# Performance work log

Measured on AMD Instinct MI355X. Metric: run time of the kernel, lower is better.

Reference implementation:

```python
import jax, jax.numpy as jnp
import numpy as np
import math

N_QUBITS = 8
EMBED_DIM = 8
NUM_HEADS = 2
N_QLAYERS = 2
TWO_PI = 2.0 * math.pi


def _apply_rx(state, theta, wire):
    # state: (N,) + (2,)*n complex64; theta: scalar or (N,)
    n = state.ndim - 1
    ax = 1 + wire
    a0 = jnp.take(state, 0, axis=ax)
    a1 = jnp.take(state, 1, axis=ax)
    half = jnp.asarray(theta) * 0.5
    c = jnp.cos(half)
    s = jnp.sin(half)
    if c.ndim:  # per-sample angle -> broadcast over remaining qubit axes
        bshape = (-1,) + (1,) * (n - 1)
        c = c.reshape(bshape)
        s = s.reshape(bshape)
    js = 1j * s
    n0 = c * a0 - js * a1
    n1 = -js * a0 + c * a1
    return jnp.stack([n0, n1], axis=ax)


def _apply_cnot(state, ctrl, tgt):
    ac, at = 1 + ctrl, 1 + tgt
    s0 = jnp.take(state, 0, axis=ac)
    s1 = jnp.take(state, 1, axis=ac)
    at2 = at - 1 if at > ac else at  # target axis index after removing control axis
    s1 = jnp.flip(s1, axis=at2)
    return jnp.stack([s0, s1], axis=ac)


def qnode(inputs, weights):
    """AngleEmbedding(RX) + BasicEntanglerLayers(RX + CNOT ring), PauliZ expvals.
    inputs: (N, n) angles; weights: (L, n). Returns (N, n) expvals, fully batched."""
    N, n = inputs.shape
    L = weights.shape[0]
    state = jnp.zeros((N,) + (2,) * n, jnp.complex64)
    state = state.at[(slice(None),) + (0,) * n].set(1.0)
    for i in range(n):  # AngleEmbedding: RX(inputs[:, i]) on wire i
        state = _apply_rx(state, inputs[:, i], i)
    for l in range(L):  # BasicEntanglerLayers
        for i in range(n):
            state = _apply_rx(state, weights[l, i], i)
        for i in range(n):
            state = _apply_cnot(state, i, (i + 1) % n)
    probs = (state.real ** 2 + state.imag ** 2).reshape(N, 2 ** n)
    # wire 0 is the most significant bit of the flattened statevector index
    idx = jnp.arange(2 ** n)
    bits = (idx[:, None] >> jnp.arange(n - 1, -1, -1)[None, :]) & 1  # (2^n, n)
    signs = (1.0 - 2.0 * bits).astype(probs.dtype)
    return probs @ signs  # (N, n)


def _qproj(x, weights):
    # apply qnode to every (batch, timestep) vector at once (vectorized loop fusion)
    B, S, E = x.shape
    return qnode(x.reshape(B * S, E), weights).reshape(B, S, E)


def _attention_forward(q, k, v, wq_w, wk_w, wv_w, wd_w):
    B, S, E = q.shape
    H, D = NUM_HEADS, EMBED_DIM // NUM_HEADS
    qp = _qproj(q, wq_w)
    kp = _qproj(k, wk_w)
    vp = _qproj(v, wv_w)
    # split heads: (B, H, S, D)
    qh = qp.reshape(B, S, H, D).transpose(0, 2, 1, 3)
    kh = kp.reshape(B, S, H, D).transpose(0, 2, 1, 3)
    vh = vp.reshape(B, S, H, D).transpose(0, 2, 1, 3)
    scores = jnp.einsum('bhqd,bhkd->bhqk', qh, kh) / jnp.sqrt(jnp.asarray(D, qh.dtype))
    attn = jax.nn.softmax(scores, axis=-1)
    ctx = jnp.einsum('bhqk,bhkd->bhqd', attn, vh)
    concat = ctx.transpose(0, 2, 1, 3).reshape(B, S, E)
    out = _qproj(concat, wd_w)
    return out, attn


def setup_inputs() -> dict:
    key = jax.random.key(0)
    kq, kk, kv, k1, k2, k3, k4 = jax.random.split(key, 7)
    B, S, E = 32, 1024, EMBED_DIM
    return {
        'q': jax.random.normal(kq, (B, S, E), jnp.float32),
        'k': jax.random.normal(kk, (B, S, E), jnp.float32),
        'v': jax.random.normal(kv, (B, S, E), jnp.float32),
        'wq_weights': jax.random.uniform(k1, (N_QLAYERS, N_QUBITS), jnp.float32) * TWO_PI,
        'wk_weights': jax.random.uniform(k2, (N_QLAYERS, N_QUBITS), jnp.float32) * TWO_PI,
        'wv_weights': jax.random.uniform(k3, (N_QLAYERS, N_QUBITS), jnp.float32) * TWO_PI,
        'dense_weights': jax.random.uniform(k4, (N_QLAYERS, N_QUBITS), jnp.float32) * TWO_PI,
    }


def reference(q, k, v, wq_weights, wk_weights, wv_weights, dense_weights):
    return _attention_forward(q, k, v, wq_weights, wk_weights, wv_weights, dense_weights)
```

## Files before the change

### kernel.cpp

```cpp
#include <hip/hip_runtime.h>
#include <math.h>


#define NSAMP 32768

typedef float f2 __attribute__((ext_vector_type(2)));

#define QX1 0xB1
#define QX2 0x4E
#define QX3 0x1B
#define QB0 0x00
#define QB1 0x55
#define QB2 0xAA
#define QB3 0xFF
#define ROW_MIRROR 0x140
#define ROW_HALF_MIRROR 0x141

template <int CTRL>
__device__ __forceinline__ float dppf(float x) {
  int xi = __float_as_int(x);
  return __int_as_float(
      __builtin_amdgcn_update_dpp(xi, xi, CTRL, 0xF, 0xF, false));
}

template <int CTRL>
__device__ __forceinline__ f2 dpp2(f2 v) {
  f2 r;
  r.x = dppf<CTRL>(v.x);
  r.y = dppf<CTRL>(v.y);
  return r;
}

__device__ __forceinline__ f2 swap2(f2 v) {
  f2 r;
  r.x = v.y;
  r.y = v.x;
  return r;
}

#define F2FMA(a, b, c) __builtin_elementwise_fma((a), (b), (c))


template <int CTRL>
__device__ __forceinline__ void gq0(float c, float s, f2* vr, f2* vi) {
  const f2 c2 = {c, c}, s2 = {s, s};
#pragma unroll
  for (int m = 0; m < 32; ++m) {
    f2 pr = dpp2<CTRL>(vr[m]);
    f2 pi = dpp2<CTRL>(vi[m]);
    vr[m] = F2FMA(c2, vr[m], s2 * pi);
    vi[m] = F2FMA(c2, vi[m], -s2 * pr);
  }
}

template <int CTRL>
__device__ __forceinline__ void gq_l1(float c, float s, f2* vr, f2* vi) {
  const f2 c2 = {c, c}, s2 = {s, s};
#pragma unroll
  for (int m = 0; m < 32; m += 2) {
    f2 pr0 = dpp2<CTRL>(vr[m]), pi0 = dpp2<CTRL>(vi[m]);
    f2 pr1 = dpp2<CTRL>(vr[m + 1]), pi1 = dpp2<CTRL>(vi[m + 1]);
    vr[m] = F2FMA(c2, vr[m], s2 * pi1);
    vi[m] = F2FMA(c2, vi[m], -s2 * pr1);
    vr[m + 1] = F2FMA(c2, vr[m + 1], s2 * pi0);
    vi[m + 1] = F2FMA(c2, vi[m + 1], -s2 * pr0);
  }
}

template <int CTRL>
__device__ __forceinline__ void gq_l20(float c, float s, f2* vr, f2* vi) {
  const f2 c2 = {c, c}, s2 = {s, s};
#pragma unroll
  for (int m = 0; m < 32; ++m) {
    f2 pr = dpp2<CTRL>(vr[m]);
    f2 pi = dpp2<CTRL>(vi[m]);
    vr[m] = F2FMA(c2, vr[m], s2 * swap2(pi));
    vi[m] = F2FMA(c2, vi[m], -s2 * swap2(pr));
  }
}

template <int ML>
__device__ __forceinline__ void gl(float c, float s, f2* vr, f2* vi) {
  constexpr int HB = ML >= 16 ? 16 : ML >= 8 ? 8 : ML >= 4 ? 4
                     : ML >= 2 ? 2 : 1;
  const f2 c2 = {c, c}, s2 = {s, s};
#pragma unroll
  for (int m = 0; m < 32; ++m) {
    if (!(m & HB)) {
      const int p = m ^ ML;
      f2 a0r = vr[m], a0i = vi[m], a1r = vr[p], a1i = vi[p];
      vr[m] = F2FMA(c2, a0r, s2 * a1i);
      vi[m] = F2FMA(c2, a0i, -s2 * a1r);
      vr[p] = F2FMA(c2, a1r, s2 * a0i);
      vi[p] = F2FMA(c2, a1i, -s2 * a0r);
    }
  }
}

__device__ __forceinline__ void gl20(float c, float s, f2* vr, f2* vi) {
  const f2 c2 = {c, c}, s2 = {s, s};
#pragma unroll
  for (int m = 0; m < 32; ++m) {
    f2 orr = vr[m], oii = vi[m];
    vr[m] = F2FMA(c2, orr, s2 * swap2(oii));
    vi[m] = F2FMA(c2, oii, -s2 * swap2(orr));
  }
}

__device__ __forceinline__ void gl30(float c, float s, f2* vr, f2* vi) {
  const f2 c2 = {c, c}, s2 = {s, s};
#pragma unroll
  for (int m = 0; m < 32; ++m) {
    if (!(m & 0x10)) {
      const int p = m ^ 0x10;
      f2 or0 = vr[m], oi0 = vi[m], or1 = vr[p], oi1 = vi[p];
      vr[m] = F2FMA(c2, or0, s2 * swap2(oi1));
      vi[m] = F2FMA(c2, oi0, -s2 * swap2(or1));
      vr[p] = F2FMA(c2, or1, s2 * swap2(oi0));
      vi[p] = F2FMA(c2, oi1, -s2 * swap2(or0));
    }
  }
}

__device__ __forceinline__ float quad_wht(float v, int qq) {
  float u = dppf<QX1>(v);
  v = (qq & 1) ? (u - v) : (v + u);
  u = dppf<QX2>(v);
  v = (qq & 2) ? (u - v) : (v + u);
  return v;
}

__device__ __forceinline__ void qsim_wave(const float* __restrict__ in,
                                          float* __restrict__ outp,
                                          int sampBase,
                                          const float* __restrict__ wc,
                                          const float* __restrict__ wsn) {
  const int lane = threadIdx.x & 63;
  const int qq = lane & 3;
  const int g = lane >> 2;
  const int samp = sampBase + g;

  const float2 xx = *(const float2*)(in + (size_t)samp * 8 + 2 * qq);
  float h0 = 0.5f * xx.x, h1 = 0.5f * xx.y;
  float c0 = cosf(h0), s0 = sinf(h0);
  float c1 = cosf(h1), s1 = sinf(h1);
  float cw[8], sw[8];
  cw[0] = dppf<QB0>(c0); cw[1] = dppf<QB0>(c1);
  sw[0] = dppf<QB0>(s0); sw[1] = dppf<QB0>(s1);
  cw[2] = dppf<QB1>(c0); cw[3] = dppf<QB1>(c1);
  sw[2] = dppf<QB1>(s0); sw[3] = dppf<QB1>(s1);
  cw[4] = dppf<QB2>(c0); cw[5] = dppf<QB2>(c1);
  sw[4] = dppf<QB2>(s0); sw[5] = dppf<QB2>(s1);
  cw[6] = dppf<QB3>(c0); cw[7] = dppf<QB3>(c1);
  sw[6] = dppf<QB3>(s0); sw[7] = dppf<QB3>(s1);

  float mm[32];
  mm[0] = ((qq & 1) ? sw[1] : cw[1]) * ((qq & 2) ? sw[0] : cw[0]);
#pragma unroll
  for (int k = 0; k < 5; ++k) {
    const float cc = cw[7 - k], ss = sw[7 - k];
#pragma unroll
    for (int t = (1 << k) - 1; t >= 0; --t) {
      mm[t + (1 << k)] = mm[t] * ss;
      mm[t] = mm[t] * cc;
    }
  }

  f2 vr[32], vi[32];
  const int pq = __builtin_popcount(qq);
#pragma unroll
  for (int m = 0; m < 32; ++m) {
    const float mx = mm[m] * cw[2];
    const float my = mm[m] * sw[2];
    const int plx = __builtin_popcount(m) & 3;
    f2 r, i;
    if (plx == 0) { r.x = mx;    i.x = 0.0f;  r.y = 0.0f;  i.y = -my; }
    else if (plx == 1) { r.x = 0.0f; i.x = -mx; r.y = -my; i.y = 0.0f; }
    else if (plx == 2) { r.x = -mx; i.x = 0.0f; r.y = 0.0f; i.y = my; }
    else { r.x = 0.0f; i.x = mx;   r.y = my;   i.y = 0.0f; }
    vr[m] = r;
    vi[m] = i;
  }
  if (pq == 1) {
#pragma unroll
    for (int m = 0; m < 32; ++m) {
      f2 t = vr[m];
      vr[m] = vi[m];
      vi[m] = -t;
    }
  } else if (pq == 2) {
#pragma unroll
    for (int m = 0; m < 32; ++m) {
      vr[m] = -vr[m];
      vi[m] = -vi[m];
    }
  }

  gq0<QX2>(wc[0], wsn[0], vr, vi);
  gq0<QX1>(wc[1], wsn[1], vr, vi);
  gl20(wc[2], wsn[2], vr, vi);
  gl<0x10>(wc[3], wsn[3], vr, vi);
  gl<0x08>(wc[4], wsn[4], vr, vi);
  gl<0x04>(wc[5], wsn[5], vr, vi);
  gl<0x02>(wc[6], wsn[6], vr, vi);
  gl<0x01>(wc[7], wsn[7], vr, vi);
  gq0<QX3>(wc[8], wsn[8], vr, vi);
  gq_l20<QX1>(wc[9], wsn[9], vr, vi);
  gl30(wc[10], wsn[10], vr, vi);
  gl<0x18>(wc[11], wsn[11], vr, vi);
  gl<0x0C>(wc[12], wsn[12], vr, vi);
  gl<0x06>(wc[13], wsn[13], vr, vi);
  gl<0x03>(wc[14], wsn[14], vr, vi);
  gq_l1<QX3>(wc[15], wsn[15], vr, vi);

  f2 wv[32];
#pragma unroll
  for (int m = 0; m < 32; ++m)
    wv[m] = F2FMA(vr[m], vr[m], vi[m] * vi[m]);
#pragma unroll
  for (int gi = 0; gi < 4; ++gi) {
#pragma unroll
    for (int k = 0; k < 3; ++k) {
#pragma unroll
      for (int j = 0; j < 8; ++j) {
        if (!(j & (1 << k))) {
          const int a = gi * 8 + j, b2 = a | (1 << k);
          f2 A = wv[a], B = wv[b2];
          wv[a] = A + B;
          wv[b2] = A - B;
        }
      }
    }
  }
  const f2 aA = (wv[5] + wv[13]) - (wv[21] + wv[29]);
  const f2 aBC = (wv[7] + wv[31]) - (wv[15] + wv[23]);
  const f2 aD = (wv[7] + wv[23]) - (wv[15] + wv[31]);
  const f2 aE = (wv[7] + wv[15]) - (wv[23] + wv[31]);
  const f2 aF = (wv[3] + wv[19]) - (wv[11] + wv[27]);
  const f2 aG = (wv[2] + wv[18]) - (wv[10] + wv[26]);
  const float accA = aA.x + aA.y;
  const float accB = aBC.x - aBC.y;
  const float accC = aBC.x + aBC.y;
  const float accD = aD.x - aD.y;
  const float accE = aE.x + aE.y;
  const float accF = aF.x - aF.y;
  const float accG = aG.x - aG.y;

  const float o15 = quad_wht(accA, qq);
  const float o3F = quad_wht(accB, qq);
  const float o1F = quad_wht(accC, qq);
  const float o2F = quad_wht(accD, qq);
  const float o17 = quad_wht(accE, qq);
  const float o2B = quad_wht(accF, qq);
  const float o2A = quad_wht(accG, qq);

  float* orow = outp + (size_t)samp * 8;
  if (qq == 3) orow[0] = o15;
  if (qq == 2) {
    orow[1] = o3F;
    orow[3] = o2F;
    orow[5] = o2B;
    orow[7] = o2A;
  }
  if (qq == 1) {
    orow[2] = o1F;
    orow[4] = o17;
    orow[6] = o15;
  }
}

__device__ __forceinline__ void weight_trig(const float* __restrict__ w,
                                            float* __restrict__ tc,
                                            float* __restrict__ tsn) {
  if (threadIdx.x < 32) {
    const int a = threadIdx.x & 15;
    const float half = 0.5f * w[a];
    if (threadIdx.x < 16)
      tc[a] = cosf(half);
    else
      tsn[a] = sinf(half);
  }
  __syncthreads();
}

__global__ __launch_bounds__(256, 2) void mhaq_qproj3_kernel(
    const float* __restrict__ q, const float* __restrict__ k,
    const float* __restrict__ v, const float* __restrict__ wq,
    const float* __restrict__ wk, const float* __restrict__ wv,
    float* __restrict__ qp, float* __restrict__ kp, float* __restrict__ vp) {
  __shared__ float tc[16], tsn[16];
  const int wg = blockIdx.x * 4 + (threadIdx.x >> 6);
  const int proj = wg >> 11;
  const float* wsel = proj == 0 ? wq : proj == 1 ? wk : wv;
  weight_trig(wsel, tc, tsn);
  const float* in = proj == 0 ? q : proj == 1 ? k : v;
  float* op = proj == 0 ? qp : proj == 1 ? kp : vp;
  qsim_wave(in, op, (wg & 2047) * 16, tc, tsn);
}

__global__ __launch_bounds__(256, 2) void mhaq_qproj1_kernel(
    const float* __restrict__ ctx, const float* __restrict__ wd,
    float* __restrict__ outp) {
  __shared__ float tc[16], tsn[16];
  weight_trig(wd, tc, tsn);
  const int wg = blockIdx.x * 4 + (threadIdx.x >> 6);
  qsim_wave(ctx, outp, wg * 16, tc, tsn);
}

__device__ __forceinline__ float wred_sum(float v) {
  v += dppf<QX1>(v);
  v += dppf<QX2>(v);
  v += dppf<ROW_HALF_MIRROR>(v);
  v += dppf<ROW_MIRROR>(v);
  v += __shfl_xor(v, 16, 64);
  v += __shfl_xor(v, 32, 64);
  return v;
}
__device__ __forceinline__ float wred_max(float v) {
  v = fmaxf(v, dppf<QX1>(v));
  v = fmaxf(v, dppf<QX2>(v));
  v = fmaxf(v, dppf<ROW_HALF_MIRROR>(v));
  v = fmaxf(v, dppf<ROW_MIRROR>(v));
  v = fmaxf(v, __shfl_xor(v, 16, 64));
  v = fmaxf(v, __shfl_xor(v, 32, 64));
  return v;
}

__global__ __launch_bounds__(256, 2) void mhaq_attn_kernel(
    const float* __restrict__ qp, const float* __restrict__ kp,
    const float* __restrict__ vp, float* __restrict__ ctx,
    float* __restrict__ attn) {
  const int wg = blockIdx.x * 4 + (threadIdx.x >> 6);
  const int bh = wg >> 7;
  const int chunk = wg & 127;
  const int b = bh >> 1, h = bh & 1;
  const int lane = threadIdx.x & 63;

  float4 kreg[16], vreg[16];
  const float* kbase = kp + (size_t)b * 1024 * 8 + h * 4;
  const float* vbase = vp + (size_t)b * 1024 * 8 + h * 4;
#pragma unroll
  for (int t = 0; t < 4; ++t) {
#pragma unroll
    for (int c = 0; c < 4; ++c) {
      const size_t j = (size_t)t * 256 + lane * 4 + c;
      kreg[t * 4 + c] = *(const float4*)(kbase + j * 8);
      vreg[t * 4 + c] = *(const float4*)(vbase + j * 8);
    }
  }

  for (int r = 0; r < 8; ++r) {
    const int i = chunk * 8 + r;
    const float4 qv = *(const float4*)(qp + ((size_t)b * 1024 + i) * 8 + h * 4);
    float e[16];
    float mx = -1e30f;
#pragma unroll
    for (int t = 0; t < 16; ++t) {
      float s = qv.x * kreg[t].x + qv.y * kreg[t].y + qv.z * kreg[t].z +
                qv.w * kreg[t].w;
      s *= 0.5f;
      e[t] = s;
      mx = fmaxf(mx, s);
    }
    mx = wred_max(mx);
    float sum = 0.0f;
#pragma unroll
    for (int t = 0; t < 16; ++t) {
      e[t] = __expf(e[t] - mx);
      sum += e[t];
    }
    sum = wred_sum(sum);
    const float rinv = 1.0f / sum;

    float a0 = 0.f, a1 = 0.f, a2 = 0.f, a3 = 0.f;
    float* arow = attn + ((size_t)(bh * 1024 + i)) * 1024;
#pragma unroll
    for (int t = 0; t < 4; ++t) {
      float p0 = e[4 * t] * rinv, p1 = e[4 * t + 1] * rinv,
            p2 = e[4 * t + 2] * rinv, p3 = e[4 * t + 3] * rinv;
      *(float4*)(arow + t * 256 + lane * 4) = make_float4(p0, p1, p2, p3);
      a0 = fmaf(p0, vreg[4 * t].x, a0);
      a1 = fmaf(p0, vreg[4 * t].y, a1);
      a2 = fmaf(p0, vreg[4 * t].z, a2);
      a3 = fmaf(p0, vreg[4 * t].w, a3);
      a0 = fmaf(p1, vreg[4 * t + 1].x, a0);
      a1 = fmaf(p1, vreg[4 * t + 1].y, a1);
      a2 = fmaf(p1, vreg[4 * t + 1].z, a2);
      a3 = fmaf(p1, vreg[4 * t + 1].w, a3);
      a0 = fmaf(p2, vreg[4 * t + 2].x, a0);
      a1 = fmaf(p2, vreg[4 * t + 2].y, a1);
      a2 = fmaf(p2, vreg[4 * t + 2].z, a2);
      a3 = fmaf(p2, vreg[4 * t + 2].w, a3);
      a0 = fmaf(p3, vreg[4 * t + 3].x, a0);
      a1 = fmaf(p3, vreg[4 * t + 3].y, a1);
      a2 = fmaf(p3, vreg[4 * t + 3].z, a2);
      a3 = fmaf(p3, vreg[4 * t + 3].w, a3);
    }
    a0 = wred_sum(a0);
    a1 = wred_sum(a1);
    a2 = wred_sum(a2);
    a3 = wred_sum(a3);
    if (lane == 0)
      *(float4*)(ctx + ((size_t)b * 1024 + i) * 8 + h * 4) =
          make_float4(a0, a1, a2, a3);
  }
}

extern "C" void kernel_launch(void* const* d_in, const int* in_sizes, int n_in,
                              void* d_out, int out_size, void* d_ws,
                              size_t ws_size, hipStream_t stream) {
  (void)in_sizes; (void)n_in; (void)out_size; (void)ws_size;
  const float* q = (const float*)d_in[0];
  const float* k = (const float*)d_in[1];
  const float* v = (const float*)d_in[2];
  const float* wq = (const float*)d_in[3];
  const float* wk = (const float*)d_in[4];
  const float* wv = (const float*)d_in[5];
  const float* wd = (const float*)d_in[6];
  float* outp = (float*)d_out;
  float* attn = outp + 262144;

  float* wsf = (float*)d_ws;
  float* qp = wsf;
  float* kp = qp + (size_t)NSAMP * 8;
  float* vp = kp + (size_t)NSAMP * 8;
  float* ctx = vp + (size_t)NSAMP * 8;

  hipLaunchKernelGGL(mhaq_qproj3_kernel, dim3(1536), dim3(256), 0, stream, q,
                     k, v, wq, wk, wv, qp, kp, vp);
  hipLaunchKernelGGL(mhaq_attn_kernel, dim3(2048), dim3(256), 0, stream, qp,
                     kp, vp, ctx, attn);
  hipLaunchKernelGGL(mhaq_qproj1_kernel, dim3(512), dim3(256), 0, stream, ctx,
                     wd, outp);
}
```

Before: 364.7 us.

## Split each 8-qubit statevector across 8 lanes instead of 4

Rewrites the quantum-projection simulation so each sample's 256 amplitudes are spread over 8 lanes with 32 scalar complex amplitudes per lane, replacing the 4-lane layout with 64 amplitudes held as float2 pairs. Cross-lane gates now use DPP permutes, including a two-step permute for the third lane bit, and the final Walsh-Hadamard reduction gains a third lane stage. Each lane now computes all eight input cosines and sines itself instead of sharing them through DPP broadcasts. Launch grids double, and launch bounds rise to 4 blocks per SIMD for lower register pressure and higher occupancy. The cost is more DPP traffic and redundant trig per lane. The attention kernel, which likely dominates runtime, is unchanged.

```diff
diff --git a/kernel.cpp b/kernel.cpp
--- a/kernel.cpp
+++ b/kernel.cpp
@@ -3,16 +3,10 @@
 
 
 #define NSAMP 32768
-
-typedef float f2 __attribute__((ext_vector_type(2)));
 
 #define QX1 0xB1
 #define QX2 0x4E
 #define QX3 0x1B
-#define QB0 0x00
-#define QB1 0x55
-#define QB2 0xAA
-#define QB3 0xFF
 #define ROW_MIRROR 0x140
 #define ROW_HALF_MIRROR 0x141
 
@@ -23,110 +17,82 @@
       __builtin_amdgcn_update_dpp(xi, xi, CTRL, 0xF, 0xF, false));
 }
 
+template <int P1>
+__device__ __forceinline__ float dpp2x(float x) {
+  return dppf<ROW_HALF_MIRROR>(dppf<P1>(x));
+}
+
+
 template <int CTRL>
-__device__ __forceinline__ f2 dpp2(f2 v) {
-  f2 r;
-  r.x = dppf<CTRL>(v.x);
-  r.y = dppf<CTRL>(v.y);
-  return r;
-}
-
-__device__ __forceinline__ f2 swap2(f2 v) {
-  f2 r;
-  r.x = v.y;
-  r.y = v.x;
-  return r;
-}
-
-#define F2FMA(a, b, c) __builtin_elementwise_fma((a), (b), (c))
-
-
-template <int CTRL>
-__device__ __forceinline__ void gq0(float c, float s, f2* vr, f2* vi) {
-  const f2 c2 = {c, c}, s2 = {s, s};
+__device__ __forceinline__ void cg1(float c, float s, float* vr, float* vi) {
 #pragma unroll
   for (int m = 0; m < 32; ++m) {
-    f2 pr = dpp2<CTRL>(vr[m]);
-    f2 pi = dpp2<CTRL>(vi[m]);
-    vr[m] = F2FMA(c2, vr[m], s2 * pi);
-    vi[m] = F2FMA(c2, vi[m], -s2 * pr);
-  }
-}
-
-template <int CTRL>
-__device__ __forceinline__ void gq_l1(float c, float s, f2* vr, f2* vi) {
-  const f2 c2 = {c, c}, s2 = {s, s};
-#pragma unroll
-  for (int m = 0; m < 32; m += 2) {
-    f2 pr0 = dpp2<CTRL>(vr[m]), pi0 = dpp2<CTRL>(vi[m]);
-    f2 pr1 = dpp2<CTRL>(vr[m + 1]), pi1 = dpp2<CTRL>(vi[m + 1]);
-    vr[m] = F2FMA(c2, vr[m], s2 * pi1);
-    vi[m] = F2FMA(c2, vi[m], -s2 * pr1);
-    vr[m + 1] = F2FMA(c2, vr[m + 1], s2 * pi0);
-    vi[m + 1] = F2FMA(c2, vi[m + 1], -s2 * pr0);
-  }
-}
-
-template <int CTRL>
-__device__ __forceinline__ void gq_l20(float c, float s, f2* vr, f2* vi) {
-  const f2 c2 = {c, c}, s2 = {s, s};
+    const float pr = dppf<CTRL>(vr[m]);
+    const float pi = dppf<CTRL>(vi[m]);
+    vr[m] = fmaf(c, vr[m], s * pi);
+    vi[m] = fmaf(c, vi[m], -s * pr);
+  }
+}
+
+template <int P1>
+__device__ __forceinline__ void cg2(float c, float s, float* vr, float* vi) {
 #pragma unroll
   for (int m = 0; m < 32; ++m) {
-    f2 pr = dpp2<CTRL>(vr[m]);
-    f2 pi = dpp2<CTRL>(vi[m]);
-    vr[m] = F2FMA(c2, vr[m], s2 * swap2(pi));
-    vi[m] = F2FMA(c2, vi[m], -s2 * swap2(pr));
-  }
-}
-
-template <int ML>
-__device__ __forceinline__ void gl(float c, float s, f2* vr, f2* vi) {
+    const float pr = dpp2x<P1>(vr[m]);
+    const float pi = dpp2x<P1>(vi[m]);
+    vr[m] = fmaf(c, vr[m], s * pi);
+    vi[m] = fmaf(c, vi[m], -s * pr);
+  }
+}
+
+template <int P1, bool TWO, int ML>
+__device__ __forceinline__ void cgl(float c, float s, float* vr, float* vi) {
   constexpr int HB = ML >= 16 ? 16 : ML >= 8 ? 8 : ML >= 4 ? 4
                      : ML >= 2 ? 2 : 1;
-  const f2 c2 = {c, c}, s2 = {s, s};
 #pragma unroll
   for (int m = 0; m < 32; ++m) {
     if (!(m & HB)) {
       const int p = m ^ ML;
-      f2 a0r = vr[m], a0i = vi[m], a1r = vr[p], a1i = vi[p];
-      vr[m] = F2FMA(c2, a0r, s2 * a1i);
-      vi[m] = F2FMA(c2, a0i, -s2 * a1r);
-      vr[p] = F2FMA(c2, a1r, s2 * a0i);
-      vi[p] = F2FMA(c2, a1i, -s2 * a0r);
-    }
-  }
-}
-
-__device__ __forceinline__ void gl20(float c, float s, f2* vr, f2* vi) {
-  const f2 c2 = {c, c}, s2 = {s, s};
+      float prl, pil, prp, pip;
+      if constexpr (TWO) {
+        prl = dpp2x<P1>(vr[p]); pil = dpp2x<P1>(vi[p]);
+        prp = dpp2x<P1>(vr[m]); pip = dpp2x<P1>(vi[m]);
+      } else {
+        prl = dppf<P1>(vr[p]); pil = dppf<P1>(vi[p]);
+        prp = dppf<P1>(vr[m]); pip = dppf<P1>(vi[m]);
+      }
+      vr[m] = fmaf(c, vr[m], s * pil);
+      vi[m] = fmaf(c, vi[m], -s * prl);
+      vr[p] = fmaf(c, vr[p], s * pip);
+      vi[p] = fmaf(c, vi[p], -s * prp);
+    }
+  }
+}
+
+template <int ML>
+__device__ __forceinline__ void gl(float c, float s, float* vr, float* vi) {
+  constexpr int HB = ML >= 16 ? 16 : ML >= 8 ? 8 : ML >= 4 ? 4
+                     : ML >= 2 ? 2 : 1;
 #pragma unroll
   for (int m = 0; m < 32; ++m) {
-    f2 orr = vr[m], oii = vi[m];
-    vr[m] = F2FMA(c2, orr, s2 * swap2(oii));
-    vi[m] = F2FMA(c2, oii, -s2 * swap2(orr));
-  }
-}
-
-__device__ __forceinline__ void gl30(float c, float s, f2* vr, f2* vi) {
-  const f2 c2 = {c, c}, s2 = {s, s};
-#pragma unroll
-  for (int m = 0; m < 32; ++m) {
-    if (!(m & 0x10)) {
-      const int p = m ^ 0x10;
-      f2 or0 = vr[m], oi0 = vi[m], or1 = vr[p], oi1 = vi[p];
-      vr[m] = F2FMA(c2, or0, s2 * swap2(oi1));
-      vi[m] = F2FMA(c2, oi0, -s2 * swap2(or1));
-      vr[p] = F2FMA(c2, or1, s2 * swap2(oi0));
-      vi[p] = F2FMA(c2, oi1, -s2 * swap2(or0));
-    }
-  }
-}
-
-__device__ __forceinline__ float quad_wht(float v, int qq) {
+    if (!(m & HB)) {
+      const int p = m ^ ML;
+      float a0r = vr[m], a0i = vi[m], a1r = vr[p], a1i = vi[p];
+      vr[m] = fmaf(c, a0r, s * a1i);
+      vi[m] = fmaf(c, a0i, -s * a1r);
+      vr[p] = fmaf(c, a1r, s * a0i);
+      vi[p] = fmaf(c, a1i, -s * a0r);
+    }
+  }
+}
+
+__device__ __forceinline__ float lane_wht8(float v, int l3) {
   float u = dppf<QX1>(v);
-  v = (qq & 1) ? (u - v) : (v + u);
+  v = (l3 & 1) ? (u - v) : (v + u);
   u = dppf<QX2>(v);
-  v = (qq & 2) ? (u - v) : (v + u);
+  v = (l3 & 2) ? (u - v) : (v + u);
+  u = dpp2x<QX3>(v);
+  v = (l3 & 4) ? (u - v) : (v + u);
   return v;
 }
 
@@ -136,29 +102,24 @@
                                           const float* __restrict__ wc,
                                           const float* __restrict__ wsn) {
   const int lane = threadIdx.x & 63;
-  const int qq = lane & 3;
-  const int g = lane >> 2;
-  const int samp = sampBase + g;
-
-  const float2 xx = *(const float2*)(in + (size_t)samp * 8 + 2 * qq);
-  float h0 = 0.5f * xx.x, h1 = 0.5f * xx.y;
-  float c0 = cosf(h0), s0 = sinf(h0);
-  float c1 = cosf(h1), s1 = sinf(h1);
-  float cw[8], sw[8];
-  cw[0] = dppf<QB0>(c0); cw[1] = dppf<QB0>(c1);
-  sw[0] = dppf<QB0>(s0); sw[1] = dppf<QB0>(s1);
-  cw[2] = dppf<QB1>(c0); cw[3] = dppf<QB1>(c1);
-  sw[2] = dppf<QB1>(s0); sw[3] = dppf<QB1>(s1);
-  cw[4] = dppf<QB2>(c0); cw[5] = dppf<QB2>(c1);
-  sw[4] = dppf<QB2>(s0); sw[5] = dppf<QB2>(s1);
-  cw[6] = dppf<QB3>(c0); cw[7] = dppf<QB3>(c1);
-  sw[6] = dppf<QB3>(s0); sw[7] = dppf<QB3>(s1);
+  const int l3 = lane & 7;
+  const int samp = sampBase + (lane >> 3);
+
+  const float* row = in + (size_t)samp * 8;
+  float ci[8], si[8];
+#pragma unroll
+  for (int w = 0; w < 8; ++w) {
+    const float half = 0.5f * row[w];
+    ci[w] = cosf(half);
+    si[w] = sinf(half);
+  }
 
   float mm[32];
-  mm[0] = ((qq & 1) ? sw[1] : cw[1]) * ((qq & 2) ? sw[0] : cw[0]);
+  mm[0] = ((l3 & 4) ? si[0] : ci[0]) * ((l3 & 2) ? si[1] : ci[1]) *
+          ((l3 & 1) ? si[2] : ci[2]);
 #pragma unroll
   for (int k = 0; k < 5; ++k) {
-    const float cc = cw[7 - k], ss = sw[7 - k];
+    const float cc = ci[7 - k], ss = si[7 - k];
 #pragma unroll
     for (int t = (1 << k) - 1; t >= 0; --t) {
       mm[t + (1 << k)] = mm[t] * ss;
@@ -166,25 +127,21 @@
     }
   }
 
-  f2 vr[32], vi[32];
-  const int pq = __builtin_popcount(qq);
+  float vr[32], vi[32];
+  const int pq = __builtin_popcount(l3) & 3;
 #pragma unroll
   for (int m = 0; m < 32; ++m) {
-    const float mx = mm[m] * cw[2];
-    const float my = mm[m] * sw[2];
-    const int plx = __builtin_popcount(m) & 3;
-    f2 r, i;
-    if (plx == 0) { r.x = mx;    i.x = 0.0f;  r.y = 0.0f;  i.y = -my; }
-    else if (plx == 1) { r.x = 0.0f; i.x = -mx; r.y = -my; i.y = 0.0f; }
-    else if (plx == 2) { r.x = -mx; i.x = 0.0f; r.y = 0.0f; i.y = my; }
-    else { r.x = 0.0f; i.x = mx;   r.y = my;   i.y = 0.0f; }
-    vr[m] = r;
-    vi[m] = i;
+    const int pl = __builtin_popcount(m) & 3;
+    const float t = mm[m];
+    if (pl == 0) { vr[m] = t;    vi[m] = 0.0f; }
+    else if (pl == 1) { vr[m] = 0.0f; vi[m] = -t; }
+    else if (pl == 2) { vr[m] = -t;   vi[m] = 0.0f; }
+    else { vr[m] = 0.0f; vi[m] = t; }
   }
   if (pq == 1) {
 #pragma unroll
     for (int m = 0; m < 32; ++m) {
-      f2 t = vr[m];
+      const float t = vr[m];
       vr[m] = vi[m];
       vi[m] = -t;
     }
@@ -194,78 +151,87 @@
       vr[m] = -vr[m];
       vi[m] = -vi[m];
     }
-  }
-
-  gq0<QX2>(wc[0], wsn[0], vr, vi);
-  gq0<QX1>(wc[1], wsn[1], vr, vi);
-  gl20(wc[2], wsn[2], vr, vi);
+  } else if (pq == 3) {
+#pragma unroll
+    for (int m = 0; m < 32; ++m) {
+      const float t = vr[m];
+      vr[m] = -vi[m];
+      vi[m] = t;
+    }
+  }
+
+  cg2<QX3>(wc[0], wsn[0], vr, vi);
+  cg1<QX2>(wc[1], wsn[1], vr, vi);
+  cg1<QX1>(wc[2], wsn[2], vr, vi);
   gl<0x10>(wc[3], wsn[3], vr, vi);
   gl<0x08>(wc[4], wsn[4], vr, vi);
   gl<0x04>(wc[5], wsn[5], vr, vi);
   gl<0x02>(wc[6], wsn[6], vr, vi);
   gl<0x01>(wc[7], wsn[7], vr, vi);
-  gq0<QX3>(wc[8], wsn[8], vr, vi);
-  gq_l20<QX1>(wc[9], wsn[9], vr, vi);
-  gl30(wc[10], wsn[10], vr, vi);
+  cg2<QX1>(wc[8], wsn[8], vr, vi);
+  cg1<QX3>(wc[9], wsn[9], vr, vi);
+  cgl<QX1, false, 0x10>(wc[10], wsn[10], vr, vi);
   gl<0x18>(wc[11], wsn[11], vr, vi);
   gl<0x0C>(wc[12], wsn[12], vr, vi);
   gl<0x06>(wc[13], wsn[13], vr, vi);
   gl<0x03>(wc[14], wsn[14], vr, vi);
-  gq_l1<QX3>(wc[15], wsn[15], vr, vi);
-
-  f2 wv[32];
-#pragma unroll
-  for (int m = 0; m < 32; ++m)
-    wv[m] = F2FMA(vr[m], vr[m], vi[m] * vi[m]);
-#pragma unroll
-  for (int gi = 0; gi < 4; ++gi) {
+  cgl<QX1, true, 0x01>(wc[15], wsn[15], vr, vi);
+
+  float accA, accB, accC, accD, accE, accF;
+#pragma unroll
+  for (int g = 0; g < 4; ++g) {
+    float w[8];
+#pragma unroll
+    for (int j = 0; j < 8; ++j) {
+      const int m = g * 8 + j;
+      w[j] = fmaf(vr[m], vr[m], vi[m] * vi[m]);
+    }
 #pragma unroll
     for (int k = 0; k < 3; ++k) {
 #pragma unroll
       for (int j = 0; j < 8; ++j) {
         if (!(j & (1 << k))) {
-          const int a = gi * 8 + j, b2 = a | (1 << k);
-          f2 A = wv[a], B = wv[b2];
-          wv[a] = A + B;
-          wv[b2] = A - B;
+          const int j2 = j | (1 << k);
+          const float a = w[j], b = w[j2];
+          w[j] = a + b;
+          w[j2] = a - b;
         }
       }
     }
-  }
-  const f2 aA = (wv[5] + wv[13]) - (wv[21] + wv[29]);
-  const f2 aBC = (wv[7] + wv[31]) - (wv[15] + wv[23]);
-  const f2 aD = (wv[7] + wv[23]) - (wv[15] + wv[31]);
-  const f2 aE = (wv[7] + wv[15]) - (wv[23] + wv[31]);
-  const f2 aF = (wv[3] + wv[19]) - (wv[11] + wv[27]);
-  const f2 aG = (wv[2] + wv[18]) - (wv[10] + wv[26]);
-  const float accA = aA.x + aA.y;
-  const float accB = aBC.x - aBC.y;
-  const float accC = aBC.x + aBC.y;
-  const float accD = aD.x - aD.y;
-  const float accE = aE.x + aE.y;
-  const float accF = aF.x - aF.y;
-  const float accG = aG.x - aG.y;
-
-  const float o15 = quad_wht(accA, qq);
-  const float o3F = quad_wht(accB, qq);
-  const float o1F = quad_wht(accC, qq);
-  const float o2F = quad_wht(accD, qq);
-  const float o17 = quad_wht(accE, qq);
-  const float o2B = quad_wht(accF, qq);
-  const float o2A = quad_wht(accG, qq);
+    if (g == 0) {
+      accA = w[5]; accB = w[7]; accC = w[7]; accD = w[7];
+      accE = w[3]; accF = w[2];
+    } else if (g == 1) {
+      accA += w[5]; accB -= w[7]; accC -= w[7]; accD += w[7];
+      accE -= w[3]; accF -= w[2];
+    } else if (g == 2) {
+      accA -= w[5]; accB -= w[7]; accC += w[7]; accD -= w[7];
+      accE += w[3]; accF += w[2];
+    } else {
+      accA -= w[5]; accB += w[7]; accC -= w[7]; accD -= w[7];
+      accE -= w[3]; accF -= w[2];
+    }
+  }
+
+  const float oA = lane_wht8(accA, l3);
+  const float oB = lane_wht8(accB, l3);
+  const float oC = lane_wht8(accC, l3);
+  const float oD = lane_wht8(accD, l3);
+  const float oE = lane_wht8(accE, l3);
+  const float oF = lane_wht8(accF, l3);
 
   float* orow = outp + (size_t)samp * 8;
-  if (qq == 3) orow[0] = o15;
-  if (qq == 2) {
-    orow[1] = o3F;
-    orow[3] = o2F;
-    orow[5] = o2B;
-    orow[7] = o2A;
-  }
-  if (qq == 1) {
-    orow[2] = o1F;
-    orow[4] = o17;
-    orow[6] = o15;
+  if (l3 == 6) orow[0] = oA;
+  if (l3 == 2) {
+    orow[2] = oB;
+    orow[4] = oD;
+    orow[6] = oA;
+  }
+  if (l3 == 5) {
+    orow[1] = oB;
+    orow[3] = oC;
+    orow[5] = oE;
+    orow[7] = oF;
   }
 }
 
@@ -283,28 +249,28 @@
   __syncthreads();
 }
 
-__global__ __launch_bounds__(256, 2) void mhaq_qproj3_kernel(
+__global__ __launch_bounds__(256, 4) void mhaq_qproj3_kernel(
     const float* __restrict__ q, const float* __restrict__ k,
     const float* __restrict__ v, const float* __restrict__ wq,
     const float* __restrict__ wk, const float* __restrict__ wv,
     float* __restrict__ qp, float* __restrict__ kp, float* __restrict__ vp) {
   __shared__ float tc[16], tsn[16];
   const int wg = blockIdx.x * 4 + (threadIdx.x >> 6);
-  const int proj = wg >> 11;
+  const int proj = wg >> 12;
   const float* wsel = proj == 0 ? wq : proj == 1 ? wk : wv;
   weight_trig(wsel, tc, tsn);
   const float* in = proj == 0 ? q : proj == 1 ? k : v;
   float* op = proj == 0 ? qp : proj == 1 ? kp : vp;
-  qsim_wave(in, op, (wg & 2047) * 16, tc, tsn);
-}
-
-__global__ __launch_bounds__(256, 2) void mhaq_qproj1_kernel(
+  qsim_wave(in, op, (wg & 4095) * 8, tc, tsn);
+}
+
+__global__ __launch_bounds__(256, 4) void mhaq_qproj1_kernel(
     const float* __restrict__ ctx, const float* __restrict__ wd,
     float* __restrict__ outp) {
   __shared__ float tc[16], tsn[16];
   weight_trig(wd, tc, tsn);
   const int wg = blockIdx.x * 4 + (threadIdx.x >> 6);
-  qsim_wave(ctx, outp, wg * 16, tc, tsn);
+  qsim_wave(ctx, outp, wg * 8, tc, tsn);
 }
 
 __device__ __forceinline__ float wred_sum(float v) {
@@ -426,10 +392,10 @@
   float* vp = kp + (size_t)NSAMP * 8;
   float* ctx = vp + (size_t)NSAMP * 8;
 
-  hipLaunchKernelGGL(mhaq_qproj3_kernel, dim3(1536), dim3(256), 0, stream, q,
+  hipLaunchKernelGGL(mhaq_qproj3_kernel, dim3(3072), dim3(256), 0, stream, q,
                      k, v, wq, wk, wv, qp, kp, vp);
   hipLaunchKernelGGL(mhaq_attn_kernel, dim3(2048), dim3(256), 0, stream, qp,
                      kp, vp, ctx, attn);
-  hipLaunchKernelGGL(mhaq_qproj1_kernel, dim3(512), dim3(256), 0, stream, ctx,
-                     wd, outp);
-}
+  hipLaunchKernelGGL(mhaq_qproj1_kernel, dim3(1024), dim3(256), 0, stream,
+                     ctx, wd, outp);
+}
```

Result: slower. 408.6 us (+12.0%).
